# Kernel tuning notes

Hardware: AMD Instinct MI355X
Metric: run time of the kernel (lower is better)

Reference implementation:

```python
import jax, jax.numpy as jnp
import numpy as np

NEG = jnp.float32(-1e30)  # max-plus identity (finite to keep grads clean)


def setup_inputs() -> dict:
    key = jax.random.key(0)
    k1, k2 = jax.random.split(key)
    B, Cin, H, W = 8, 64, 64, 64
    Cout, kH, kW = 64, 3, 3
    x = jax.random.normal(k1, (B, Cin, H, W), dtype=jnp.float32)
    weight = jax.random.normal(k2, (Cout, Cin, kH, kW), dtype=jnp.float32)
    return {"x": x, "weight": weight, "kernel_size": 3, "padding": 1}


def reference(x, weight, kernel_size, padding):
    # Max-plus correlation (tropical conv), stride 1:
    #   out[b,co,y,x] = max_{ci,i,j} ( x_pad[b,ci,y+i,x+j] + weight[co,ci,i,j] )
    kH = kW = int(kernel_size)
    padH = padW = int(padding)
    B, Cin, H, W = x.shape
    Cout = weight.shape[0]
    xp = jnp.pad(x, ((0, 0), (0, 0), (padH, padH), (padW, padW)),
                 constant_values=NEG)  # -inf-like padding: identity of max
    Ho = H + 2 * padH - kH + 1
    Wo = W + 2 * padW - kW + 1
    out = jnp.full((B, Cout, Ho, Wo), NEG, dtype=x.dtype)
    for i in range(kH):          # small fixed kernel loop (kH*kW taps)
        for j in range(kW):
            win = xp[:, :, i:i + Ho, j:j + Wo]            # [B,Ci,Ho,Wo]
            cand = win[:, None] + weight[None, :, :, i, j, None, None]
            out = jnp.maximum(out, cand.max(axis=2))      # reduce over Ci
    return out
```

## Files before the change

### kernel.cpp

```cpp
#include <hip/hip_runtime.h>

#define NEGV -1e30f

constexpr int Bn = 8, Ci = 64, Hn = 64, Wn = 64, Co = 64;

constexpr int COB = 8;
constexpr int HT  = 8;
constexpr int XROWS = HT + 2;
constexpr int XCOLS = Wn + 2;
constexpr int XTILE = XROWS * XCOLS;

__global__ __launch_bounds__(256, 2)
void maxconv_kernel(const float* __restrict__ x, const float* __restrict__ wt,
                    float* __restrict__ out) {
    __shared__ float xs[2][XROWS][XCOLS];

    const int tid = threadIdx.x;
    const int h0  = blockIdx.x * HT;
    const int co0 = blockIdx.y * COB;
    const int b   = blockIdx.z;

    const int r  = tid >> 5;
    const int wi = (tid & 31) * 2;

    const float* xb = x + (size_t)b * Ci * Hn * Wn;

    int srow[3], scol[3];
    bool sact[3];
    float sreg[3];
#pragma unroll
    for (int k = 0; k < 3; k++) {
        int idx = tid + k * 256;
        sact[k] = (idx < XTILE);
        srow[k] = idx / XCOLS;
        scol[k] = idx % XCOLS;
    }

    auto stage_load = [&](int ci) {
#pragma unroll
        for (int k = 0; k < 3; k++) {
            float v = NEGV;
            if (sact[k]) {
                int gh = h0 - 1 + srow[k];
                int gw = scol[k] - 1;
                if (gh >= 0 && gh < Hn && gw >= 0 && gw < Wn)
                    v = xb[((size_t)ci * Hn + gh) * Wn + gw];
            }
            sreg[k] = v;
        }
    };
    auto stage_store = [&](int buf) {
#pragma unroll
        for (int k = 0; k < 3; k++) {
            if (sact[k])
                (&xs[buf][0][0])[srow[k] * XCOLS + scol[k]] = sreg[k];
        }
    };

    float acc[COB][2];
#pragma unroll
    for (int c = 0; c < COB; c++) { acc[c][0] = NEGV; acc[c][1] = NEGV; }

    stage_load(0);
    stage_store(0);
    __syncthreads();

    for (int ci = 0; ci < Ci; ci++) {
        const int buf = ci & 1;
        if (ci + 1 < Ci) stage_load(ci + 1);

        float xv[3][4];
#pragma unroll
        for (int i = 0; i < 3; i++) {
            const float2* rowp = (const float2*)&xs[buf][r + i][wi];
            float2 a = rowp[0];
            float2 bb = rowp[1];
            xv[i][0] = a.x; xv[i][1] = a.y; xv[i][2] = bb.x; xv[i][3] = bb.y;
        }

#pragma unroll
        for (int c = 0; c < COB; c++) {
            const float* wp = wt + ((size_t)(co0 + c) * Ci + ci) * 9;
            float w0 = wp[0], w1 = wp[1], w2 = wp[2];
            float w3 = wp[3], w4 = wp[4], w5 = wp[5];
            float w6 = wp[6], w7 = wp[7], w8 = wp[8];
#pragma unroll
            for (int p = 0; p < 2; p++) {
                float t0 = xv[0][p + 0] + w0;
                float t1 = xv[0][p + 1] + w1;
                float t2 = xv[0][p + 2] + w2;
                float t3 = xv[1][p + 0] + w3;
                float t4 = xv[1][p + 1] + w4;
                float t5 = xv[1][p + 2] + w5;
                float t6 = xv[2][p + 0] + w6;
                float t7 = xv[2][p + 1] + w7;
                float t8 = xv[2][p + 2] + w8;
                float a = acc[c][p];
                a = fmaxf(a, fmaxf(t0, t1));
                a = fmaxf(a, fmaxf(t2, t3));
                a = fmaxf(a, fmaxf(t4, t5));
                a = fmaxf(a, fmaxf(t6, t7));
                a = fmaxf(a, t8);
                acc[c][p] = a;
            }
        }

        if (ci + 1 < Ci) stage_store((ci + 1) & 1);
        __syncthreads();
    }

#pragma unroll
    for (int c = 0; c < COB; c++) {
        size_t o = (((size_t)b * Co + co0 + c) * Hn + (h0 + r)) * Wn + wi;
        float2 v = make_float2(acc[c][0], acc[c][1]);
        *(float2*)(out + o) = v;
    }
}

extern "C" void kernel_launch(void* const* d_in, const int* in_sizes, int n_in,
                              void* d_out, int out_size, void* d_ws, size_t ws_size,
                              hipStream_t stream) {
    const float* x  = (const float*)d_in[0];
    const float* wt = (const float*)d_in[1];
    float* out = (float*)d_out;

    dim3 grid(Hn / HT, Co / COB, Bn);
    maxconv_kernel<<<grid, 256, 0, stream>>>(x, wt, out);
}
```

Baseline: 136.6 us.

## Drop LDS staging; read conv halo directly from global via cache

Removes the double-buffered shared-memory tile and its per-channel barriers. Each 64-lane wave now computes one output row, reading its 3x3 neighborhood straight from global memory, and leans on L1/L2 to supply the overlapping loads. Each thread now produces one output pixel per channel block instead of two, and the grid is reordered so that channel-blocks sharing the same input rows launch adjacently. The cost is roughly nine global loads per thread per input channel instead of shared-memory reuse, plus less register reuse of the loaded input values.

```diff
diff --git a/kernel.cpp b/kernel.cpp
--- a/kernel.cpp
+++ b/kernel.cpp
@@ -5,115 +5,65 @@
 constexpr int Bn = 8, Ci = 64, Hn = 64, Wn = 64, Co = 64;
 
 constexpr int COB = 8;
-constexpr int HT  = 8;
-constexpr int XROWS = HT + 2;
-constexpr int XCOLS = Wn + 2;
-constexpr int XTILE = XROWS * XCOLS;
+constexpr int HT  = 4;
 
-__global__ __launch_bounds__(256, 2)
+__global__ __launch_bounds__(256, 4)
 void maxconv_kernel(const float* __restrict__ x, const float* __restrict__ wt,
                     float* __restrict__ out) {
-    __shared__ float xs[2][XROWS][XCOLS];
+    const int lane = threadIdx.x & 63;
+    const int wrow = threadIdx.x >> 6;
+    const int co0  = blockIdx.x * COB;
+    const int h    = blockIdx.y * HT + wrow;
+    const int b    = blockIdx.z;
 
-    const int tid = threadIdx.x;
-    const int h0  = blockIdx.x * HT;
-    const int co0 = blockIdx.y * COB;
-    const int b   = blockIdx.z;
+    const int cl = lane > 0      ? lane - 1 : 0;
+    const int cr = lane < Wn - 1 ? lane + 1 : Wn - 1;
+    const bool edgeL = (lane == 0);
+    const bool edgeR = (lane == Wn - 1);
+    const bool hasUp = (h > 0);
+    const bool hasDn = (h < Hn - 1);
 
-    const int r  = tid >> 5;
-    const int wi = (tid & 31) * 2;
+    float acc[COB];
+#pragma unroll
+    for (int c = 0; c < COB; c++) acc[c] = NEGV;
 
-    const float* xb = x + (size_t)b * Ci * Hn * Wn;
+    const float* p = x + ((size_t)b * Ci * Hn + h) * Wn;
 
-    int srow[3], scol[3];
-    bool sact[3];
-    float sreg[3];
-#pragma unroll
-    for (int k = 0; k < 3; k++) {
-        int idx = tid + k * 256;
-        sact[k] = (idx < XTILE);
-        srow[k] = idx / XCOLS;
-        scol[k] = idx % XCOLS;
-    }
+    for (int ci = 0; ci < Ci; ci++, p += Hn * Wn) {
+        float lm1 = NEGV, xm1 = NEGV, rm1 = NEGV;
+        float lp1 = NEGV, xp1 = NEGV, rp1 = NEGV;
+        if (hasUp) { lm1 = p[cl - Wn]; xm1 = p[lane - Wn]; rm1 = p[cr - Wn]; }
+        if (hasDn) { lp1 = p[cl + Wn]; xp1 = p[lane + Wn]; rp1 = p[cr + Wn]; }
+        float l0 = p[cl], x0 = p[lane], r0 = p[cr];
 
-    auto stage_load = [&](int ci) {
-#pragma unroll
-        for (int k = 0; k < 3; k++) {
-            float v = NEGV;
-            if (sact[k]) {
-                int gh = h0 - 1 + srow[k];
-                int gw = scol[k] - 1;
-                if (gh >= 0 && gh < Hn && gw >= 0 && gw < Wn)
-                    v = xb[((size_t)ci * Hn + gh) * Wn + gw];
-            }
-            sreg[k] = v;
-        }
-    };
-    auto stage_store = [&](int buf) {
-#pragma unroll
-        for (int k = 0; k < 3; k++) {
-            if (sact[k])
-                (&xs[buf][0][0])[srow[k] * XCOLS + scol[k]] = sreg[k];
-        }
-    };
-
-    float acc[COB][2];
-#pragma unroll
-    for (int c = 0; c < COB; c++) { acc[c][0] = NEGV; acc[c][1] = NEGV; }
-
-    stage_load(0);
-    stage_store(0);
-    __syncthreads();
-
-    for (int ci = 0; ci < Ci; ci++) {
-        const int buf = ci & 1;
-        if (ci + 1 < Ci) stage_load(ci + 1);
-
-        float xv[3][4];
-#pragma unroll
-        for (int i = 0; i < 3; i++) {
-            const float2* rowp = (const float2*)&xs[buf][r + i][wi];
-            float2 a = rowp[0];
-            float2 bb = rowp[1];
-            xv[i][0] = a.x; xv[i][1] = a.y; xv[i][2] = bb.x; xv[i][3] = bb.y;
-        }
+        if (edgeL) { lm1 = NEGV; l0 = NEGV; lp1 = NEGV; }
+        if (edgeR) { rm1 = NEGV; r0 = NEGV; rp1 = NEGV; }
 
 #pragma unroll
         for (int c = 0; c < COB; c++) {
             const float* wp = wt + ((size_t)(co0 + c) * Ci + ci) * 9;
-            float w0 = wp[0], w1 = wp[1], w2 = wp[2];
-            float w3 = wp[3], w4 = wp[4], w5 = wp[5];
-            float w6 = wp[6], w7 = wp[7], w8 = wp[8];
-#pragma unroll
-            for (int p = 0; p < 2; p++) {
-                float t0 = xv[0][p + 0] + w0;
-                float t1 = xv[0][p + 1] + w1;
-                float t2 = xv[0][p + 2] + w2;
-                float t3 = xv[1][p + 0] + w3;
-                float t4 = xv[1][p + 1] + w4;
-                float t5 = xv[1][p + 2] + w5;
-                float t6 = xv[2][p + 0] + w6;
-                float t7 = xv[2][p + 1] + w7;
-                float t8 = xv[2][p + 2] + w8;
-                float a = acc[c][p];
-                a = fmaxf(a, fmaxf(t0, t1));
-                a = fmaxf(a, fmaxf(t2, t3));
-                a = fmaxf(a, fmaxf(t4, t5));
-                a = fmaxf(a, fmaxf(t6, t7));
-                a = fmaxf(a, t8);
-                acc[c][p] = a;
-            }
+            float t0 = lm1 + wp[0];
+            float t1 = xm1 + wp[1];
+            float t2 = rm1 + wp[2];
+            float t3 = l0  + wp[3];
+            float t4 = x0  + wp[4];
+            float t5 = r0  + wp[5];
+            float t6 = lp1 + wp[6];
+            float t7 = xp1 + wp[7];
+            float t8 = rp1 + wp[8];
+            float a = acc[c];
+            a = fmaxf(a, fmaxf(t0, t1));
+            a = fmaxf(a, fmaxf(t2, t3));
+            a = fmaxf(a, fmaxf(t4, t5));
+            a = fmaxf(a, fmaxf(t6, t7));
+            a = fmaxf(a, t8);
+            acc[c] = a;
         }
-
-        if (ci + 1 < Ci) stage_store((ci + 1) & 1);
-        __syncthreads();
     }
 
 #pragma unroll
     for (int c = 0; c < COB; c++) {
-        size_t o = (((size_t)b * Co + co0 + c) * Hn + (h0 + r)) * Wn + wi;
-        float2 v = make_float2(acc[c][0], acc[c][1]);
-        *(float2*)(out + o) = v;
+        out[(((size_t)b * Co + co0 + c) * Hn + h) * Wn + lane] = acc[c];
     }
 }
 
@@ -124,6 +74,6 @@
     const float* wt = (const float*)d_in[1];
     float* out = (float*)d_out;
 
-    dim3 grid(Hn / HT, Co / COB, Bn);
+    dim3 grid(Co / COB, Hn / HT, Bn);
     maxconv_kernel<<<grid, 256, 0, stream>>>(x, wt, out);
 }
```

New measurement: 124.9 us. 1.09x faster.
